# Performance work log

Hardware: AMD Instinct MI355X
Metric: run time of the kernel (lower is better)

Reference implementation:

```python
import jax, jax.numpy as jnp
import numpy as np

N = 100000        # nodes
E = 3200000       # edges
F_IN = 512        # node features
H = 64            # hidden (self.hidden)
C = 40            # num_class
CONF_R = 0.5      # global conf_r threshold ratio
EPS = 1e-8        # torch cosine_similarity eps


def setup_inputs() -> dict:
    key = jax.random.key(0)
    ks = jax.random.split(key, 8)
    x = jax.random.normal(ks[0], (N, F_IN), dtype=jnp.float32)
    edge_index = jax.random.randint(ks[1], (2, E), 0, N, dtype=jnp.int32)
    edge_weight = jax.random.uniform(ks[2], (E,), dtype=jnp.float32)
    l_u_edges = jax.random.uniform(ks[3], (E,), dtype=jnp.float32)
    w1 = jax.random.normal(ks[4], (F_IN, H), dtype=jnp.float32) / np.float32(np.sqrt(F_IN))
    b1 = jnp.zeros((H,), dtype=jnp.float32)
    w2 = jax.random.normal(ks[5], (H, C), dtype=jnp.float32) / np.float32(np.sqrt(H))
    b2 = jnp.zeros((C,), dtype=jnp.float32)
    return {"x": x, "edge_index": edge_index, "edge_weight": edge_weight,
            "l_u_edges": l_u_edges, "w1": w1, "b1": b1, "w2": w2, "b2": b2}


def _gcn_propagate(h, src, dst, deg_inv_sqrt):
    # GCNConv symmetric normalization with self-loops:
    # out[i] = sum_{j->i} h[j] / sqrt(deg_j * deg_i) + h[i] / deg_i
    norm = deg_inv_sqrt[src] * deg_inv_sqrt[dst]          # [E]
    agg = jax.ops.segment_sum(h[src] * norm[:, None], dst, num_segments=N)
    agg = agg + h * (deg_inv_sqrt * deg_inv_sqrt)[:, None]  # self-loop term
    return agg


def reference(x, edge_index, edge_weight, l_u_edges, w1, b1, w2, b2):
    src = edge_index[0]
    dst = edge_index[1]
    # degree with self-loops (GCNConv default add_self_loops=True, unit edge weight)
    deg = jax.ops.segment_sum(jnp.ones((E,), x.dtype), dst, num_segments=N) + 1.0
    deg_inv_sqrt = jax.lax.rsqrt(deg)

    # layer 1: linear -> propagate -> bias -> relu  (dropout treated as identity/eval)
    h1 = _gcn_propagate(x @ w1, src, dst, deg_inv_sqrt) + b1
    h1 = jax.nn.relu(h1)
    # layer 2
    x2 = _gcn_propagate(h1 @ w2, src, dst, deg_inv_sqrt) + b2   # [N, C]

    # loss path: top-k threshold on edge_weight
    n_cut = int(E * CONF_R)
    thresh = jnp.sort(edge_weight)[E - n_cut]   # n_cut-th largest value

    a = x2[src]                                  # [E, C] gather
    b = x2[dst]
    na = jnp.maximum(jnp.sqrt(jnp.sum(a * a, axis=1)), EPS)
    nb = jnp.maximum(jnp.sqrt(jnp.sum(b * b, axis=1)), EPS)
    cos = jnp.sum(a * b, axis=1) / (na * nb)
    cosine_sim = 1.0 - cos

    mask = edge_weight >= thresh
    l_prop = jnp.where(mask, cosine_sim, 1.0 - cosine_sim)
    l_edge = jnp.where(mask, edge_weight, 1.0 - edge_weight)
    l_loss = jnp.mean(l_edge * l_prop * l_u_edges)   # data_id != 5 -> mean

    return jax.nn.log_softmax(x2, axis=1), l_loss
```

## Files before the change

kernel.cpp:

```cpp
#include <hip/hip_runtime.h>

#define NN 100000
#define NE 3200000
#define FIN 512
#define FH 64
#define FC 40
#define KRANK 1600000u
#define HBLK 512
#define HBINS 2048
#define NBUCK 782
#define BPAD 1024
#define SBLK 500
#define EPB 6400
#define LEPT 4

typedef __attribute__((ext_vector_type(8))) short bf16x8;
typedef __attribute__((ext_vector_type(4))) float f32x4;

__device__ __forceinline__ unsigned f2b_rn(float x) {
    unsigned u = __float_as_uint(x);
    return (u + 0x7FFFu + ((u >> 16) & 1u)) >> 16;
}
__device__ __forceinline__ unsigned pack2(float x, float y) {
    return f2b_rn(x) | (f2b_rn(y) << 16);
}
__device__ __forceinline__ float2 unp2(unsigned u) {
    return make_float2(__uint_as_float(u << 16), __uint_as_float(u & 0xFFFF0000u));
}
__device__ __forceinline__ int dot4i8(unsigned a, unsigned b, int c) {
    c += ((int)(a << 24) >> 24) * ((int)(b << 24) >> 24);
    c += ((int)(a << 16) >> 24) * ((int)(b << 16) >> 24);
    c += ((int)(a << 8) >> 24) * ((int)(b << 8) >> 24);
    c += ((int)a >> 24) * ((int)b >> 24);
    return c;
}

__global__ __launch_bounds__(256) void bucket_count(const int* __restrict__ dstv,
                                                    unsigned* __restrict__ bcnt) {
    __shared__ unsigned bh[4 * BPAD];
    int tid = threadIdx.x, wv = tid >> 6;
    for (int i = tid; i < 4 * BPAD; i += 256) bh[i] = 0u;
    __syncthreads();
    int base = blockIdx.x * EPB;
    for (int t = tid; t < EPB; t += 256) {
        int b = dstv[base + t] >> 7;
        atomicAdd(&bh[wv * BPAD + b], 1u);
    }
    __syncthreads();
    for (int i = tid; i < BPAD; i += 256) {
        unsigned s = bh[i] + bh[BPAD + i] + bh[2 * BPAD + i] + bh[3 * BPAD + i];
        if (s) atomicAdd(&bcnt[i], s);
    }
}

__global__ __launch_bounds__(1024) void bucket_scan(const unsigned* __restrict__ bcnt,
                                                    unsigned* __restrict__ boff,
                                                    unsigned* __restrict__ bfill,
                                                    int* __restrict__ row_ptr) {
    __shared__ unsigned sc[1024];
    int tid = threadIdx.x;
    unsigned v = (tid < NBUCK) ? bcnt[tid] : 0u;
    sc[tid] = v;
    __syncthreads();
    for (int off = 1; off < 1024; off <<= 1) {
        unsigned t = (tid >= off) ? sc[tid - off] : 0u;
        __syncthreads();
        sc[tid] += t;
        __syncthreads();
    }
    unsigned excl = sc[tid] - v;
    boff[tid] = excl;
    bfill[tid] = excl;
    if (tid == 0) row_ptr[NN] = NE;
}

__global__ __launch_bounds__(256) void bucket_scatter(const int* __restrict__ srcv,
                                                      const int* __restrict__ dstv,
                                                      unsigned* __restrict__ bfill,
                                                      unsigned* __restrict__ bp) {
    __shared__ unsigned bh[4 * BPAD];
    __shared__ unsigned bbase[BPAD];
    __shared__ unsigned bfl[BPAD];
    int tid = threadIdx.x, wv = tid >> 6;
    for (int i = tid; i < 4 * BPAD; i += 256) bh[i] = 0u;
    __syncthreads();
    int base = blockIdx.x * EPB;
    for (int t = tid; t < EPB; t += 256) {
        int b = dstv[base + t] >> 7;
        atomicAdd(&bh[wv * BPAD + b], 1u);
    }
    __syncthreads();
    for (int i = tid; i < BPAD; i += 256) {
        unsigned s = bh[i] + bh[BPAD + i] + bh[2 * BPAD + i] + bh[3 * BPAD + i];
        bbase[i] = s ? atomicAdd(&bfill[i], s) : 0u;
        bfl[i] = 0u;
    }
    __syncthreads();
    for (int t = tid; t < EPB; t += 256) {
        int d = dstv[base + t];
        int b = d >> 7;
        unsigned r = atomicAdd(&bfl[b], 1u);
        unsigned pk = (unsigned)srcv[base + t] | ((unsigned)(d & 127) << 17);
        bp[bbase[b] + r] = pk;
    }
}

__global__ __launch_bounds__(256) void bucket_build(const unsigned* __restrict__ bp,
                                                    const unsigned* __restrict__ boff,
                                                    int* __restrict__ row_ptr,
                                                    float* __restrict__ dis,
                                                    int* __restrict__ csr_src) {
    __shared__ unsigned lh[4 * 128];
    __shared__ unsigned sc[128];
    __shared__ unsigned gbase[128];
    __shared__ unsigned fl2[128];
    int b = blockIdx.x, tid = threadIdx.x, wv = tid >> 6;
    unsigned e0 = boff[b], e1 = boff[b + 1];
    int ecnt = (int)(e1 - e0);
    for (int i = tid; i < 512; i += 256) lh[i] = 0u;
    __syncthreads();
    for (int t = tid; t < ecnt; t += 256) {
        unsigned lid = bp[e0 + t] >> 17;
        atomicAdd(&lh[wv * 128 + lid], 1u);
    }
    __syncthreads();
    unsigned deg = 0;
    if (tid < 128) {
        deg = lh[tid] + lh[128 + tid] + lh[256 + tid] + lh[384 + tid];
        sc[tid] = deg;
    }
    __syncthreads();
    for (int off = 1; off < 128; off <<= 1) {
        unsigned t = (tid >= off && tid < 128) ? sc[tid - off] : 0u;
        __syncthreads();
        if (tid < 128) sc[tid] += t;
        __syncthreads();
    }
    if (tid < 128) {
        unsigned excl = sc[tid] - deg;
        gbase[tid] = e0 + excl;
        fl2[tid] = 0u;
        int n = b * 128 + tid;
        if (n < NN) {
            row_ptr[n] = (int)(e0 + excl);
            dis[n] = rsqrtf((float)deg + 1.0f);
        }
    }
    __syncthreads();
    for (int t = tid; t < ecnt; t += 256) {
        unsigned v = bp[e0 + t];
        unsigned lid = v >> 17;
        unsigned r = atomicAdd(&fl2[lid], 1u);
        csr_src[gbase[lid] + r] = (int)(v & 0x1FFFFu);
    }
}

__global__ __launch_bounds__(256) void hist_pass(const float* __restrict__ ew,
                                                 const int* __restrict__ sel,
                                                 int stage,
                                                 unsigned* __restrict__ hist) {
    __shared__ unsigned lh[4 * HBINS];
    int tid = threadIdx.x, blk = blockIdx.x;
    int wv = tid >> 6;
    for (int i = tid; i < 4 * HBINS; i += 256) lh[i] = 0u;
    __syncthreads();
    unsigned m1 = 0, m2 = 0;
    if (stage == 1) m1 = (unsigned)sel[0];
    if (stage == 2) m2 = ((unsigned)sel[0] << 11) | (unsigned)sel[2];
    int base = blk * (NE / HBLK);
    for (int t = tid; t < NE / HBLK; t += 256) {
        unsigned bits = __float_as_uint(ew[base + t]);
        if (stage == 0) {
            atomicAdd(&lh[wv * HBINS + (bits >> 21)], 1u);
        } else if (stage == 1) {
            if ((bits >> 21) == m1) atomicAdd(&lh[wv * HBINS + ((bits >> 10) & 0x7FFu)], 1u);
        } else {
            if ((bits >> 10) == m2) atomicAdd(&lh[wv * HBINS + (bits & 0x3FFu)], 1u);
        }
    }
    __syncthreads();
    for (int i = tid; i < HBINS; i += 256) {
        unsigned s = lh[i] + lh[HBINS + i] + lh[2 * HBINS + i] + lh[3 * HBINS + i];
        if (s) atomicAdd(&hist[i], s);
    }
}

__global__ __launch_bounds__(1024) void select_stage(unsigned* __restrict__ hist,
                                                     int* __restrict__ sel, int stage,
                                                     float* __restrict__ thr) {
    __shared__ unsigned sc[1024];
    __shared__ unsigned runs;
    int tid = threadIdx.x;
    unsigned Kr = (stage == 0) ? KRANK : (unsigned)sel[2 * stage - 1];
    if (tid == 0) runs = 0;
    __syncthreads();
    for (int ch = 0; ch < 2; ++ch) {
        unsigned v = hist[ch * 1024 + tid];
        sc[tid] = v;
        __syncthreads();
        for (int off = 1; off < 1024; off <<= 1) {
            unsigned t = (tid >= off) ? sc[tid - off] : 0u;
            __syncthreads();
            sc[tid] += t;
            __syncthreads();
        }
        unsigned incl = sc[tid];
        unsigned base = runs;
        unsigned lo = base + incl - v, hi = base + incl;
        if (Kr >= lo && Kr < hi) {
            int b = ch * 1024 + tid;
            sel[2 * stage] = b;
            sel[2 * stage + 1] = (int)(Kr - lo);
            if (stage == 2) {
                unsigned bits = ((unsigned)sel[0] << 21) | ((unsigned)sel[2] << 10) | (unsigned)b;
                thr[0] = __uint_as_float(bits);
            }
        }
        __syncthreads();
        if (tid == 1023) runs = base + incl;
        __syncthreads();
    }
    hist[tid] = 0u;
    hist[1024 + tid] = 0u;
}

__global__ __launch_bounds__(256) void gemm1(const float* __restrict__ x,
                                             const float* __restrict__ w1,
                                             unsigned short* __restrict__ hb) {
    __shared__ unsigned sA[64 * 20];
    __shared__ unsigned sB[64 * 20];
    int tid = threadIdx.x;
    int wv = tid >> 6, lane = tid & 63;
    int quad = lane >> 4, l16 = lane & 15;
    int rowBase = blockIdx.x * 64;
    f32x4 acc[4] = {};
    for (int k0 = 0; k0 < FIN; k0 += 32) {
#pragma unroll
        for (int i = 0; i < 2; ++i) {
            int idx = tid + 256 * i;
            int m = idx >> 3, q = idx & 7;
            int gr = rowBase + m;
            float4 v = (gr < NN) ? *(const float4*)&x[(size_t)gr * FIN + k0 + 4 * q]
                                 : make_float4(0.f, 0.f, 0.f, 0.f);
            sA[m * 20 + 2 * q] = pack2(v.x, v.y);
            sA[m * 20 + 2 * q + 1] = pack2(v.z, v.w);
        }
#pragma unroll
        for (int i = 0; i < 4; ++i) {
            int idx = tid + 256 * i;
            int n = idx & 63, kk = idx >> 6;
            float a = w1[(size_t)(k0 + 2 * kk) * FH + n];
            float b = w1[(size_t)(k0 + 2 * kk + 1) * FH + n];
            sB[n * 20 + kk] = pack2(a, b);
        }
        __syncthreads();
        bf16x8 af = *(const bf16x8*)&sA[(wv * 16 + l16) * 20 + quad * 4];
#pragma unroll
        for (int c = 0; c < 4; ++c) {
            bf16x8 bfg = *(const bf16x8*)&sB[(c * 16 + l16) * 20 + quad * 4];
            acc[c] = __builtin_amdgcn_mfma_f32_16x16x32_bf16(af, bfg, acc[c], 0, 0, 0);
        }
        __syncthreads();
    }
#pragma unroll
    for (int r = 0; r < 4; ++r) {
        int row = rowBase + wv * 16 + quad * 4 + r;
        if (row < NN) {
#pragma unroll
            for (int c = 0; c < 4; ++c)
                hb[(size_t)row * FH + c * 16 + l16] = (unsigned short)f2b_rn(acc[c][r]);
        }
    }
}

__global__ __launch_bounds__(256) void agg_relu1(const unsigned* __restrict__ hbw,
                                                 const float* __restrict__ dis,
                                                 const int* __restrict__ row_ptr,
                                                 const int* __restrict__ csr_src,
                                                 const float* __restrict__ b1,
                                                 float* __restrict__ h1) {
    int wave = threadIdx.x >> 6, lane = threadIdx.x & 63;
    int n = blockIdx.x * 4 + wave;
    if (n >= NN) return;
    int g = lane >> 3, j = lane & 7;
    float dn = dis[n];
    int e0 = row_ptr[n], e1 = row_ptr[n + 1];
    int total = e1 - e0 + 1;
    const uint4* hb4 = (const uint4*)hbw;
    float2 a0 = {0.f, 0.f}, a1 = {0.f, 0.f}, a2 = {0.f, 0.f}, a3 = {0.f, 0.f};
    for (int it = 0; it < total; it += 16) {
        int iA = it + g;
        int iB = it + 8 + g;
        int sA = n;
        float wA = 0.f;
        if (iA == 0) {
            wA = dn * dn;
        } else if (iA < total) {
            sA = csr_src[e0 + iA - 1];
            wA = dis[sA] * dn;
        }
        int sB = n;
        float wB = 0.f;
        if (iB < total) {
            sB = csr_src[e0 + iB - 1];
            wB = dis[sB] * dn;
        }
        uint4 vA = make_uint4(0u, 0u, 0u, 0u);
        uint4 vB = make_uint4(0u, 0u, 0u, 0u);
        if (iA < total) vA = hb4[(size_t)sA * 8 + j];
        if (iB < total) vB = hb4[(size_t)sB * 8 + j];
        float2 t;
        t = unp2(vA.x); a0.x = fmaf(t.x, wA, a0.x); a0.y = fmaf(t.y, wA, a0.y);
        t = unp2(vA.y); a1.x = fmaf(t.x, wA, a1.x); a1.y = fmaf(t.y, wA, a1.y);
        t = unp2(vA.z); a2.x = fmaf(t.x, wA, a2.x); a2.y = fmaf(t.y, wA, a2.y);
        t = unp2(vA.w); a3.x = fmaf(t.x, wA, a3.x); a3.y = fmaf(t.y, wA, a3.y);
        t = unp2(vB.x); a0.x = fmaf(t.x, wB, a0.x); a0.y = fmaf(t.y, wB, a0.y);
        t = unp2(vB.y); a1.x = fmaf(t.x, wB, a1.x); a1.y = fmaf(t.y, wB, a1.y);
        t = unp2(vB.z); a2.x = fmaf(t.x, wB, a2.x); a2.y = fmaf(t.y, wB, a2.y);
        t = unp2(vB.w); a3.x = fmaf(t.x, wB, a3.x); a3.y = fmaf(t.y, wB, a3.y);
    }
#pragma unroll
    for (int m = 8; m < 64; m <<= 1) {
        a0.x += __shfl_xor(a0.x, m); a0.y += __shfl_xor(a0.y, m);
        a1.x += __shfl_xor(a1.x, m); a1.y += __shfl_xor(a1.y, m);
        a2.x += __shfl_xor(a2.x, m); a2.y += __shfl_xor(a2.y, m);
        a3.x += __shfl_xor(a3.x, m); a3.y += __shfl_xor(a3.y, m);
    }
    if (g == 0) {
        float4 blo = *(const float4*)&b1[j * 8];
        float4 bhi = *(const float4*)&b1[j * 8 + 4];
        float4 olo = make_float4(fmaxf(a0.x + blo.x, 0.f), fmaxf(a0.y + blo.y, 0.f),
                                 fmaxf(a1.x + blo.z, 0.f), fmaxf(a1.y + blo.w, 0.f));
        float4 ohi = make_float4(fmaxf(a2.x + bhi.x, 0.f), fmaxf(a2.y + bhi.y, 0.f),
                                 fmaxf(a3.x + bhi.z, 0.f), fmaxf(a3.y + bhi.w, 0.f));
        *(float4*)&h1[(size_t)n * FH + j * 8] = olo;
        *(float4*)&h1[(size_t)n * FH + j * 8 + 4] = ohi;
    }
}

__global__ __launch_bounds__(256) void gemm2(const float* __restrict__ h1,
                                             const float* __restrict__ w2,
                                             unsigned* __restrict__ h2w) {
    __shared__ float w2s[FH * FC];
    int tid = threadIdx.x;
    for (int i = tid; i < FH * FC; i += 256) w2s[i] = w2[i];
    __syncthreads();
    int wave = tid >> 6, lane = tid & 63;
    int n = blockIdx.x * 4 + wave;
    if (n >= NN) return;
    float hv = h1[(size_t)n * FH + lane];
    int cl = (lane < FC) ? lane : 0;
    float acc = 0.f;
#pragma unroll
    for (int k = 0; k < FH; ++k) {
        float xk = __shfl(hv, k);
        acc = fmaf(xk, w2s[k * FC + cl], acc);
    }
    float lo = __shfl(acc, 2 * lane);
    float hi = __shfl(acc, 2 * lane + 1);
    if (lane < 20) h2w[(size_t)n * 20 + lane] = pack2(lo, hi);
}

__global__ __launch_bounds__(256) void agg2_fused(const unsigned* __restrict__ h2w,
                                                  const float* __restrict__ dis,
                                                  const int* __restrict__ row_ptr,
                                                  const int* __restrict__ csr_src,
                                                  const float* __restrict__ b2,
                                                  unsigned* __restrict__ x2b,
                                                  float* __restrict__ outls) {
    int wave = threadIdx.x >> 6, lane = threadIdx.x & 63;
    int n = blockIdx.x * 4 + wave;
    if (n >= NN) return;
    int half = lane >> 5, li = lane & 31;
    bool ld = li < 20;
    int lidx = ld ? li : 19;
    float dn = dis[n];
    float2 acc = make_float2(0.f, 0.f);
    if (half == 0 && ld) {
        float2 v = unp2(h2w[(size_t)n * 20 + li]);
        float w = dn * dn;
        acc.x = v.x * w; acc.y = v.y * w;
    }
    int e0 = row_ptr[n], e1 = row_ptr[n + 1];
    int e = e0 + half;
    for (; e + 6 < e1; e += 8) {
        int s0 = csr_src[e], s1 = csr_src[e + 2];
        int s2 = csr_src[e + 4], s3 = csr_src[e + 6];
        float w0 = dis[s0] * dn, w1w = dis[s1] * dn;
        float w2w = dis[s2] * dn, w3w = dis[s3] * dn;
        float2 v0 = unp2(h2w[(size_t)s0 * 20 + lidx]);
        float2 v1 = unp2(h2w[(size_t)s1 * 20 + lidx]);
        float2 v2 = unp2(h2w[(size_t)s2 * 20 + lidx]);
        float2 v3 = unp2(h2w[(size_t)s3 * 20 + lidx]);
        if (ld) {
            acc.x = fmaf(v0.x, w0, acc.x); acc.y = fmaf(v0.y, w0, acc.y);
            acc.x = fmaf(v1.x, w1w, acc.x); acc.y = fmaf(v1.y, w1w, acc.y);
            acc.x = fmaf(v2.x, w2w, acc.x); acc.y = fmaf(v2.y, w2w, acc.y);
            acc.x = fmaf(v3.x, w3w, acc.x); acc.y = fmaf(v3.y, w3w, acc.y);
        }
    }
    for (; e + 2 < e1; e += 4) {
        int s0 = csr_src[e], s1 = csr_src[e + 2];
        float w0 = dis[s0] * dn, w1w = dis[s1] * dn;
        float2 v0 = unp2(h2w[(size_t)s0 * 20 + lidx]);
        float2 v1 = unp2(h2w[(size_t)s1 * 20 + lidx]);
        if (ld) {
            acc.x = fmaf(v0.x, w0, acc.x); acc.y = fmaf(v0.y, w0, acc.y);
            acc.x = fmaf(v1.x, w1w, acc.x); acc.y = fmaf(v1.y, w1w, acc.y);
        }
    }
    if (e < e1) {
        int s = csr_src[e];
        float w = dis[s] * dn;
        float2 v = unp2(h2w[(size_t)s * 20 + lidx]);
        if (ld) { acc.x = fmaf(v.x, w, acc.x); acc.y = fmaf(v.y, w, acc.y); }
    }
    float ax = acc.x + __shfl_xor(acc.x, 32);
    float ay = acc.y + __shfl_xor(acc.y, 32);
    bool actv = (half == 0) && ld;
    float2 x2v;
    if (actv) {
        float2 b = ((const float2*)b2)[li];
        x2v = make_float2(ax + b.x, ay + b.y);
    } else {
        x2v = make_float2(-3.4e38f, -3.4e38f);
    }
    float m = fmaxf(x2v.x, x2v.y);
#pragma unroll
    for (int off = 16; off; off >>= 1) m = fmaxf(m, __shfl_xor(m, off));
    float ex = actv ? (expf(x2v.x - m) + expf(x2v.y - m)) : 0.f;
    float sq = actv ? (x2v.x * x2v.x + x2v.y * x2v.y) : 0.f;
#pragma unroll
    for (int off = 16; off; off >>= 1) {
        ex += __shfl_xor(ex, off);
        sq += __shfl_xor(sq, off);
    }
    unsigned pk = 0;
    float inv = 0.f;
    if (actv) {
        inv = 127.f / fmaxf(sqrtf(sq), 1e-8f);
        int qx = (int)rintf(fminf(fmaxf(x2v.x * inv, -127.f), 127.f));
        int qy = (int)rintf(fminf(fmaxf(x2v.y * inv, -127.f), 127.f));
        pk = (unsigned)(qx & 0xFF) | ((unsigned)(qy & 0xFF) << 8);
    }
    unsigned wlo = __shfl(pk, (2 * lane) & 63);
    unsigned whi = __shfl(pk, (2 * lane + 1) & 63);
    unsigned wrd = wlo | (whi << 16);
    if (lane < 12) x2b[(size_t)n * 12 + lane] = wrd;
    if (actv) {
        float lse = m + logf(ex);
        *(float2*)&outls[(size_t)n * FC + 2 * li] = make_float2(x2v.x - lse, x2v.y - lse);
    }
}

__global__ __launch_bounds__(256) void loss_kernel(const int* __restrict__ srcv,
                                                   const int* __restrict__ dstv,
                                                   const float* __restrict__ ew,
                                                   const float* __restrict__ lu,
                                                   const unsigned* __restrict__ x2b,
                                                   const float* __restrict__ thr,
                                                   double* __restrict__ acc) {
    int base = blockIdx.x * (256 * LEPT) + threadIdx.x;
    float thr0 = thr[0];
    int s[LEPT], d[LEPT];
    float w[LEPT], l[LEPT];
#pragma unroll
    for (int i = 0; i < LEPT; ++i) {
        int e = base + i * 256;
        s[i] = srcv[e];
        d[i] = dstv[e];
        w[i] = ew[e];
        l[i] = lu[e];
    }
    uint4 A[LEPT][3], B[LEPT][3];
#pragma unroll
    for (int i = 0; i < LEPT; ++i) {
        const uint4* pa = (const uint4*)(x2b + (size_t)s[i] * 12);
        const uint4* pb = (const uint4*)(x2b + (size_t)d[i] * 12);
#pragma unroll
        for (int j = 0; j < 3; ++j) {
            A[i][j] = pa[j];
            B[i][j] = pb[j];
        }
    }
    float term = 0.f;
#pragma unroll
    for (int i = 0; i < LEPT; ++i) {
        int dot = 0;
#pragma unroll
        for (int j = 0; j < 3; ++j) {
            uint4 av = A[i][j], bv = B[i][j];
            dot = dot4i8(av.x, bv.x, dot);
            dot = dot4i8(av.y, bv.y, dot);
            dot = dot4i8(av.z, bv.z, dot);
            dot = dot4i8(av.w, bv.w, dot);
        }
        float cosv = (float)dot * (1.0f / 16129.0f);
        float cs = 1.f - cosv;
        bool mk = (w[i] >= thr0);
        float lp = mk ? cs : 1.f - cs;
        float le = mk ? w[i] : 1.f - w[i];
        term = fmaf(le * lp, l[i], term);
    }
#pragma unroll
    for (int off = 32; off; off >>= 1) term += __shfl_down(term, off);
    __shared__ float ws4[4];
    int lane = threadIdx.x & 63, wid = threadIdx.x >> 6;
    if (lane == 0) ws4[wid] = term;
    __syncthreads();
    if (threadIdx.x == 0) {
        double sm = (double)ws4[0] + (double)ws4[1] + (double)ws4[2] + (double)ws4[3];
        atomicAdd(acc, sm);
    }
}

__global__ void finalize(const double* __restrict__ acc, float* __restrict__ out) {
    out[NN * FC] = (float)(acc[0] * (1.0 / (double)NE));
}

extern "C" void kernel_launch(void* const* d_in, const int* in_sizes, int n_in,
                              void* d_out, int out_size, void* d_ws, size_t ws_size,
                              hipStream_t stream) {
    const float* x  = (const float*)d_in[0];
    const int*   ei = (const int*)d_in[1];
    const float* ew = (const float*)d_in[2];
    const float* lu = (const float*)d_in[3];
    const float* w1 = (const float*)d_in[4];
    const float* b1 = (const float*)d_in[5];
    const float* w2 = (const float*)d_in[6];
    const float* b2 = (const float*)d_in[7];
    float* out = (float*)d_out;
    const int* srcv = ei;
    const int* dstv = ei + NE;

    char* ws = (char*)d_ws;
    size_t off = 0;
    auto alloc = [&](size_t bytes) -> void* {
        void* p = ws + off;
        off += (bytes + 255) & ~(size_t)255;
        return p;
    };
    float*    dis     = (float*)alloc((size_t)NN * 4);
    int*      row_ptr = (int*)alloc((size_t)(NN + 1) * 4);
    int*      csr_src = (int*)alloc((size_t)NE * 4);
    unsigned* bp      = (unsigned*)alloc((size_t)NE * 4);
    unsigned* bcnt    = (unsigned*)alloc((size_t)BPAD * 4);
    unsigned* boff2   = (unsigned*)alloc((size_t)BPAD * 4);
    unsigned* bfill   = (unsigned*)alloc((size_t)BPAD * 4);
    unsigned short* hb = (unsigned short*)alloc((size_t)NN * FH * 2);
    float*    h1      = (float*)alloc((size_t)NN * FH * 4);
    unsigned* h2w     = (unsigned*)alloc((size_t)NN * 20 * 4);
    unsigned* x2b     = (unsigned*)alloc((size_t)NN * 12 * 4);
    unsigned* histr   = (unsigned*)alloc((size_t)HBINS * 4);
    int*      sel     = (int*)alloc(256);
    float*    thr     = (float*)alloc(256);
    double*   accd    = (double*)alloc(256);

    hipMemsetAsync(bcnt, 0, (size_t)BPAD * 4, stream);
    hipMemsetAsync(histr, 0, (size_t)HBINS * 4, stream);
    hipMemsetAsync(accd, 0, 8, stream);

    const int LB = NE / (256 * LEPT);
    const int NB4 = (NN + 3) / 4;

    bucket_count<<<SBLK, 256, 0, stream>>>(dstv, bcnt);
    bucket_scan<<<1, 1024, 0, stream>>>(bcnt, boff2, bfill, row_ptr);
    bucket_scatter<<<SBLK, 256, 0, stream>>>(srcv, dstv, bfill, bp);
    bucket_build<<<NBUCK, 256, 0, stream>>>(bp, boff2, row_ptr, dis, csr_src);

    hist_pass<<<HBLK, 256, 0, stream>>>(ew, sel, 0, histr);
    select_stage<<<1, 1024, 0, stream>>>(histr, sel, 0, thr);
    hist_pass<<<HBLK, 256, 0, stream>>>(ew, sel, 1, histr);
    select_stage<<<1, 1024, 0, stream>>>(histr, sel, 1, thr);
    hist_pass<<<HBLK, 256, 0, stream>>>(ew, sel, 2, histr);
    select_stage<<<1, 1024, 0, stream>>>(histr, sel, 2, thr);

    gemm1<<<(NN + 63) / 64, 256, 0, stream>>>(x, w1, hb);
    agg_relu1<<<NB4, 256, 0, stream>>>((const unsigned*)hb, dis, row_ptr, csr_src, b1, h1);
    gemm2<<<NB4, 256, 0, stream>>>(h1, w2, h2w);
    agg2_fused<<<NB4, 256, 0, stream>>>(h2w, dis, row_ptr, csr_src, b2, x2b, out);
    loss_kernel<<<LB, 256, 0, stream>>>(srcv, dstv, ew, lu, x2b, thr, accd);
    finalize<<<1, 1, 0, stream>>>(accd, out);
}
```

Before: 926.5 us.

## Restructure gemm1, widen aggregation unrolling, pad layer-2 features to 64-byte rows

gemm1 now stages all of w1 in shared memory once per block and loads x rows straight from global into MFMA operand registers. Each wave computes 32 rows with two accumulator sets, which removes the per-k-step shared staging of x and its barriers. The layer-1 aggregation now issues four neighbour gathers per iteration instead of two, for more memory-level parallelism. The layer-2 features are padded to 32 words (bf16) and 16 words (int8), so agg2 can reuse the same 8-lane uint4 gather pattern and the loss kernel can do aligned loads. This trades extra memory footprint and padded traffic for wider, aligned gathers.

```diff
diff --git a/kernel.cpp b/kernel.cpp
--- a/kernel.cpp
+++ b/kernel.cpp
@@ -227,48 +227,57 @@
 __global__ __launch_bounds__(256) void gemm1(const float* __restrict__ x,
                                              const float* __restrict__ w1,
                                              unsigned short* __restrict__ hb) {
-    __shared__ unsigned sA[64 * 20];
-    __shared__ unsigned sB[64 * 20];
+    __shared__ unsigned sB[64 * 260];
     int tid = threadIdx.x;
+    {
+        int col = tid & 63;
+        for (int kw = tid >> 6; kw < 256; kw += 4) {
+            float a = w1[(size_t)(2 * kw) * FH + col];
+            float b = w1[(size_t)(2 * kw + 1) * FH + col];
+            sB[col * 260 + kw] = pack2(a, b);
+        }
+    }
+    __syncthreads();
     int wv = tid >> 6, lane = tid & 63;
-    int quad = lane >> 4, l16 = lane & 15;
-    int rowBase = blockIdx.x * 64;
-    f32x4 acc[4] = {};
+    int l16 = lane & 15, quad = lane >> 4;
+    int r0 = blockIdx.x * 128 + wv * 32;
+    int rowA = r0 + l16, rowB = r0 + 16 + l16;
+    bool okA = rowA < NN, okB = rowB < NN;
+    const float* pA = x + (size_t)(okA ? rowA : 0) * FIN + quad * 8;
+    const float* pB = x + (size_t)(okB ? rowB : 0) * FIN + quad * 8;
+    f32x4 accA[4] = {};
+    f32x4 accB[4] = {};
     for (int k0 = 0; k0 < FIN; k0 += 32) {
-#pragma unroll
-        for (int i = 0; i < 2; ++i) {
-            int idx = tid + 256 * i;
-            int m = idx >> 3, q = idx & 7;
-            int gr = rowBase + m;
-            float4 v = (gr < NN) ? *(const float4*)&x[(size_t)gr * FIN + k0 + 4 * q]
-                                 : make_float4(0.f, 0.f, 0.f, 0.f);
-            sA[m * 20 + 2 * q] = pack2(v.x, v.y);
-            sA[m * 20 + 2 * q + 1] = pack2(v.z, v.w);
-        }
-#pragma unroll
-        for (int i = 0; i < 4; ++i) {
-            int idx = tid + 256 * i;
-            int n = idx & 63, kk = idx >> 6;
-            float a = w1[(size_t)(k0 + 2 * kk) * FH + n];
-            float b = w1[(size_t)(k0 + 2 * kk + 1) * FH + n];
-            sB[n * 20 + kk] = pack2(a, b);
-        }
-        __syncthreads();
-        bf16x8 af = *(const bf16x8*)&sA[(wv * 16 + l16) * 20 + quad * 4];
+        float4 xa0 = *(const float4*)(pA + k0);
+        float4 xa1 = *(const float4*)(pA + k0 + 4);
+        float4 xb0 = *(const float4*)(pB + k0);
+        float4 xb1 = *(const float4*)(pB + k0 + 4);
+        union { unsigned u[4]; bf16x8 v; } ca, cb;
+        ca.u[0] = pack2(xa0.x, xa0.y); ca.u[1] = pack2(xa0.z, xa0.w);
+        ca.u[2] = pack2(xa1.x, xa1.y); ca.u[3] = pack2(xa1.z, xa1.w);
+        cb.u[0] = pack2(xb0.x, xb0.y); cb.u[1] = pack2(xb0.z, xb0.w);
+        cb.u[2] = pack2(xb1.x, xb1.y); cb.u[3] = pack2(xb1.z, xb1.w);
+        int kwb = (k0 >> 1) + quad * 4;
 #pragma unroll
         for (int c = 0; c < 4; ++c) {
-            bf16x8 bfg = *(const bf16x8*)&sB[(c * 16 + l16) * 20 + quad * 4];
-            acc[c] = __builtin_amdgcn_mfma_f32_16x16x32_bf16(af, bfg, acc[c], 0, 0, 0);
-        }
-        __syncthreads();
+            bf16x8 bf = *(const bf16x8*)&sB[(c * 16 + l16) * 260 + kwb];
+            accA[c] = __builtin_amdgcn_mfma_f32_16x16x32_bf16(ca.v, bf, accA[c], 0, 0, 0);
+            accB[c] = __builtin_amdgcn_mfma_f32_16x16x32_bf16(cb.v, bf, accB[c], 0, 0, 0);
+        }
     }
 #pragma unroll
     for (int r = 0; r < 4; ++r) {
-        int row = rowBase + wv * 16 + quad * 4 + r;
-        if (row < NN) {
+        int rowc = r0 + quad * 4 + r;
+        if (rowc < NN) {
 #pragma unroll
             for (int c = 0; c < 4; ++c)
-                hb[(size_t)row * FH + c * 16 + l16] = (unsigned short)f2b_rn(acc[c][r]);
+                hb[(size_t)rowc * FH + c * 16 + l16] = (unsigned short)f2b_rn(accA[c][r]);
+        }
+        int rowd = r0 + 16 + quad * 4 + r;
+        if (rowd < NN) {
+#pragma unroll
+            for (int c = 0; c < 4; ++c)
+                hb[(size_t)rowd * FH + c * 16 + l16] = (unsigned short)f2b_rn(accB[c][r]);
         }
     }
 }
@@ -288,36 +297,30 @@
     int total = e1 - e0 + 1;
     const uint4* hb4 = (const uint4*)hbw;
     float2 a0 = {0.f, 0.f}, a1 = {0.f, 0.f}, a2 = {0.f, 0.f}, a3 = {0.f, 0.f};
-    for (int it = 0; it < total; it += 16) {
-        int iA = it + g;
-        int iB = it + 8 + g;
-        int sA = n;
-        float wA = 0.f;
-        if (iA == 0) {
-            wA = dn * dn;
-        } else if (iA < total) {
-            sA = csr_src[e0 + iA - 1];
-            wA = dis[sA] * dn;
-        }
-        int sB = n;
-        float wB = 0.f;
-        if (iB < total) {
-            sB = csr_src[e0 + iB - 1];
-            wB = dis[sB] * dn;
-        }
-        uint4 vA = make_uint4(0u, 0u, 0u, 0u);
-        uint4 vB = make_uint4(0u, 0u, 0u, 0u);
-        if (iA < total) vA = hb4[(size_t)sA * 8 + j];
-        if (iB < total) vB = hb4[(size_t)sB * 8 + j];
+    for (int it = 0; it < total; it += 32) {
+        int i0 = it + g, i1 = i0 + 8, i2 = i0 + 16, i3 = i0 + 24;
+        int s0 = n, s1 = n, s2 = n, s3 = n;
+        if (i0 > 0 && i0 < total) s0 = csr_src[e0 + i0 - 1];
+        if (i1 < total) s1 = csr_src[e0 + i1 - 1];
+        if (i2 < total) s2 = csr_src[e0 + i2 - 1];
+        if (i3 < total) s3 = csr_src[e0 + i3 - 1];
+        float w0 = (i0 < total) ? ((i0 == 0) ? dn * dn : dis[s0] * dn) : 0.f;
+        float w1_ = (i1 < total) ? dis[s1] * dn : 0.f;
+        float w2_ = (i2 < total) ? dis[s2] * dn : 0.f;
+        float w3_ = (i3 < total) ? dis[s3] * dn : 0.f;
+        uint4 z4 = make_uint4(0u, 0u, 0u, 0u);
+        uint4 v0 = z4, v1 = z4, v2 = z4, v3 = z4;
+        if (i0 < total) v0 = hb4[(size_t)s0 * 8 + j];
+        if (i1 < total) v1 = hb4[(size_t)s1 * 8 + j];
+        if (i2 < total) v2 = hb4[(size_t)s2 * 8 + j];
+        if (i3 < total) v3 = hb4[(size_t)s3 * 8 + j];
         float2 t;
-        t = unp2(vA.x); a0.x = fmaf(t.x, wA, a0.x); a0.y = fmaf(t.y, wA, a0.y);
-        t = unp2(vA.y); a1.x = fmaf(t.x, wA, a1.x); a1.y = fmaf(t.y, wA, a1.y);
-        t = unp2(vA.z); a2.x = fmaf(t.x, wA, a2.x); a2.y = fmaf(t.y, wA, a2.y);
-        t = unp2(vA.w); a3.x = fmaf(t.x, wA, a3.x); a3.y = fmaf(t.y, wA, a3.y);
-        t = unp2(vB.x); a0.x = fmaf(t.x, wB, a0.x); a0.y = fmaf(t.y, wB, a0.y);
-        t = unp2(vB.y); a1.x = fmaf(t.x, wB, a1.x); a1.y = fmaf(t.y, wB, a1.y);
-        t = unp2(vB.z); a2.x = fmaf(t.x, wB, a2.x); a2.y = fmaf(t.y, wB, a2.y);
-        t = unp2(vB.w); a3.x = fmaf(t.x, wB, a3.x); a3.y = fmaf(t.y, wB, a3.y);
+#define ACC8(V, W)                                                     \
+        t = unp2(V.x); a0.x = fmaf(t.x, W, a0.x); a0.y = fmaf(t.y, W, a0.y); \
+        t = unp2(V.y); a1.x = fmaf(t.x, W, a1.x); a1.y = fmaf(t.y, W, a1.y); \
+        t = unp2(V.z); a2.x = fmaf(t.x, W, a2.x); a2.y = fmaf(t.y, W, a2.y); \
+        t = unp2(V.w); a3.x = fmaf(t.x, W, a3.x); a3.y = fmaf(t.y, W, a3.y);
+        ACC8(v0, w0) ACC8(v1, w1_) ACC8(v2, w2_) ACC8(v3, w3_)
     }
 #pragma unroll
     for (int m = 8; m < 64; m <<= 1) {
@@ -356,9 +359,9 @@
         float xk = __shfl(hv, k);
         acc = fmaf(xk, w2s[k * FC + cl], acc);
     }
-    float lo = __shfl(acc, 2 * lane);
-    float hi = __shfl(acc, 2 * lane + 1);
-    if (lane < 20) h2w[(size_t)n * 20 + lane] = pack2(lo, hi);
+    float lo = __shfl(acc, (2 * lane) & 63);
+    float hi = __shfl(acc, (2 * lane + 1) & 63);
+    if (lane < 32) h2w[(size_t)n * 32 + lane] = (lane < 20) ? pack2(lo, hi) : 0u;
 }
 
 __global__ __launch_bounds__(256) void agg2_fused(const unsigned* __restrict__ h2w,
@@ -371,85 +374,87 @@
     int wave = threadIdx.x >> 6, lane = threadIdx.x & 63;
     int n = blockIdx.x * 4 + wave;
     if (n >= NN) return;
-    int half = lane >> 5, li = lane & 31;
-    bool ld = li < 20;
-    int lidx = ld ? li : 19;
+    int g = lane >> 3, j = lane & 7;
     float dn = dis[n];
-    float2 acc = make_float2(0.f, 0.f);
-    if (half == 0 && ld) {
-        float2 v = unp2(h2w[(size_t)n * 20 + li]);
-        float w = dn * dn;
-        acc.x = v.x * w; acc.y = v.y * w;
-    }
     int e0 = row_ptr[n], e1 = row_ptr[n + 1];
-    int e = e0 + half;
-    for (; e + 6 < e1; e += 8) {
-        int s0 = csr_src[e], s1 = csr_src[e + 2];
-        int s2 = csr_src[e + 4], s3 = csr_src[e + 6];
-        float w0 = dis[s0] * dn, w1w = dis[s1] * dn;
-        float w2w = dis[s2] * dn, w3w = dis[s3] * dn;
-        float2 v0 = unp2(h2w[(size_t)s0 * 20 + lidx]);
-        float2 v1 = unp2(h2w[(size_t)s1 * 20 + lidx]);
-        float2 v2 = unp2(h2w[(size_t)s2 * 20 + lidx]);
-        float2 v3 = unp2(h2w[(size_t)s3 * 20 + lidx]);
-        if (ld) {
-            acc.x = fmaf(v0.x, w0, acc.x); acc.y = fmaf(v0.y, w0, acc.y);
-            acc.x = fmaf(v1.x, w1w, acc.x); acc.y = fmaf(v1.y, w1w, acc.y);
-            acc.x = fmaf(v2.x, w2w, acc.x); acc.y = fmaf(v2.y, w2w, acc.y);
-            acc.x = fmaf(v3.x, w3w, acc.x); acc.y = fmaf(v3.y, w3w, acc.y);
-        }
-    }
-    for (; e + 2 < e1; e += 4) {
-        int s0 = csr_src[e], s1 = csr_src[e + 2];
-        float w0 = dis[s0] * dn, w1w = dis[s1] * dn;
-        float2 v0 = unp2(h2w[(size_t)s0 * 20 + lidx]);
-        float2 v1 = unp2(h2w[(size_t)s1 * 20 + lidx]);
-        if (ld) {
-            acc.x = fmaf(v0.x, w0, acc.x); acc.y = fmaf(v0.y, w0, acc.y);
-            acc.x = fmaf(v1.x, w1w, acc.x); acc.y = fmaf(v1.y, w1w, acc.y);
-        }
-    }
-    if (e < e1) {
-        int s = csr_src[e];
-        float w = dis[s] * dn;
-        float2 v = unp2(h2w[(size_t)s * 20 + lidx]);
-        if (ld) { acc.x = fmaf(v.x, w, acc.x); acc.y = fmaf(v.y, w, acc.y); }
-    }
-    float ax = acc.x + __shfl_xor(acc.x, 32);
-    float ay = acc.y + __shfl_xor(acc.y, 32);
-    bool actv = (half == 0) && ld;
-    float2 x2v;
-    if (actv) {
-        float2 b = ((const float2*)b2)[li];
-        x2v = make_float2(ax + b.x, ay + b.y);
-    } else {
-        x2v = make_float2(-3.4e38f, -3.4e38f);
-    }
-    float m = fmaxf(x2v.x, x2v.y);
-#pragma unroll
-    for (int off = 16; off; off >>= 1) m = fmaxf(m, __shfl_xor(m, off));
-    float ex = actv ? (expf(x2v.x - m) + expf(x2v.y - m)) : 0.f;
-    float sq = actv ? (x2v.x * x2v.x + x2v.y * x2v.y) : 0.f;
-#pragma unroll
-    for (int off = 16; off; off >>= 1) {
+    int total = e1 - e0 + 1;
+    const uint4* h4 = (const uint4*)h2w;
+    float2 a0 = {0.f, 0.f}, a1 = {0.f, 0.f}, a2 = {0.f, 0.f}, a3 = {0.f, 0.f};
+    for (int it = 0; it < total; it += 32) {
+        int i0 = it + g, i1 = i0 + 8, i2 = i0 + 16, i3 = i0 + 24;
+        int s0 = n, s1 = n, s2 = n, s3 = n;
+        if (i0 > 0 && i0 < total) s0 = csr_src[e0 + i0 - 1];
+        if (i1 < total) s1 = csr_src[e0 + i1 - 1];
+        if (i2 < total) s2 = csr_src[e0 + i2 - 1];
+        if (i3 < total) s3 = csr_src[e0 + i3 - 1];
+        float w0 = (i0 < total) ? ((i0 == 0) ? dn * dn : dis[s0] * dn) : 0.f;
+        float w1_ = (i1 < total) ? dis[s1] * dn : 0.f;
+        float w2_ = (i2 < total) ? dis[s2] * dn : 0.f;
+        float w3_ = (i3 < total) ? dis[s3] * dn : 0.f;
+        uint4 z4 = make_uint4(0u, 0u, 0u, 0u);
+        uint4 v0 = z4, v1 = z4, v2 = z4, v3 = z4;
+        if (i0 < total) v0 = h4[(size_t)s0 * 8 + j];
+        if (i1 < total) v1 = h4[(size_t)s1 * 8 + j];
+        if (i2 < total) v2 = h4[(size_t)s2 * 8 + j];
+        if (i3 < total) v3 = h4[(size_t)s3 * 8 + j];
+        float2 t;
+        ACC8(v0, w0) ACC8(v1, w1_) ACC8(v2, w2_) ACC8(v3, w3_)
+    }
+#pragma unroll
+    for (int m = 8; m < 64; m <<= 1) {
+        a0.x += __shfl_xor(a0.x, m); a0.y += __shfl_xor(a0.y, m);
+        a1.x += __shfl_xor(a1.x, m); a1.y += __shfl_xor(a1.y, m);
+        a2.x += __shfl_xor(a2.x, m); a2.y += __shfl_xor(a2.y, m);
+        a3.x += __shfl_xor(a3.x, m); a3.y += __shfl_xor(a3.y, m);
+    }
+    bool jv = (j < 5);
+    float4 blo = make_float4(0.f, 0.f, 0.f, 0.f), bhi = blo;
+    if (jv) {
+        blo = *(const float4*)&b2[j * 8];
+        bhi = *(const float4*)&b2[j * 8 + 4];
+    }
+    float c0 = a0.x + blo.x, c1 = a0.y + blo.y, c2 = a1.x + blo.z, c3 = a1.y + blo.w;
+    float c4 = a2.x + bhi.x, c5 = a2.y + bhi.y, c6 = a3.x + bhi.z, c7 = a3.y + bhi.w;
+    if (!jv) { c0 = c1 = c2 = c3 = c4 = c5 = c6 = c7 = -3.4e38f; }
+    float mx = fmaxf(fmaxf(fmaxf(c0, c1), fmaxf(c2, c3)),
+                     fmaxf(fmaxf(c4, c5), fmaxf(c6, c7)));
+#pragma unroll
+    for (int off = 1; off < 8; off <<= 1) mx = fmaxf(mx, __shfl_xor(mx, off));
+    float ex = 0.f, sq = 0.f;
+    if (jv) {
+        ex = expf(c0 - mx) + expf(c1 - mx) + expf(c2 - mx) + expf(c3 - mx)
+           + expf(c4 - mx) + expf(c5 - mx) + expf(c6 - mx) + expf(c7 - mx);
+        sq = c0 * c0 + c1 * c1 + c2 * c2 + c3 * c3 + c4 * c4 + c5 * c5 + c6 * c6 + c7 * c7;
+    }
+#pragma unroll
+    for (int off = 1; off < 8; off <<= 1) {
         ex += __shfl_xor(ex, off);
         sq += __shfl_xor(sq, off);
     }
-    unsigned pk = 0;
-    float inv = 0.f;
-    if (actv) {
-        inv = 127.f / fmaxf(sqrtf(sq), 1e-8f);
-        int qx = (int)rintf(fminf(fmaxf(x2v.x * inv, -127.f), 127.f));
-        int qy = (int)rintf(fminf(fmaxf(x2v.y * inv, -127.f), 127.f));
-        pk = (unsigned)(qx & 0xFF) | ((unsigned)(qy & 0xFF) << 8);
-    }
-    unsigned wlo = __shfl(pk, (2 * lane) & 63);
-    unsigned whi = __shfl(pk, (2 * lane + 1) & 63);
-    unsigned wrd = wlo | (whi << 16);
-    if (lane < 12) x2b[(size_t)n * 12 + lane] = wrd;
-    if (actv) {
-        float lse = m + logf(ex);
-        *(float2*)&outls[(size_t)n * FC + 2 * li] = make_float2(x2v.x - lse, x2v.y - lse);
+    if (g == 0) {
+        if (jv) {
+            float inv = 127.f / fmaxf(sqrtf(sq), 1e-8f);
+            int q0 = (int)rintf(fminf(fmaxf(c0 * inv, -127.f), 127.f));
+            int q1 = (int)rintf(fminf(fmaxf(c1 * inv, -127.f), 127.f));
+            int q2 = (int)rintf(fminf(fmaxf(c2 * inv, -127.f), 127.f));
+            int q3 = (int)rintf(fminf(fmaxf(c3 * inv, -127.f), 127.f));
+            int q4 = (int)rintf(fminf(fmaxf(c4 * inv, -127.f), 127.f));
+            int q5 = (int)rintf(fminf(fmaxf(c5 * inv, -127.f), 127.f));
+            int q6 = (int)rintf(fminf(fmaxf(c6 * inv, -127.f), 127.f));
+            int q7 = (int)rintf(fminf(fmaxf(c7 * inv, -127.f), 127.f));
+            unsigned qlo = (unsigned)(q0 & 255) | ((unsigned)(q1 & 255) << 8) |
+                           ((unsigned)(q2 & 255) << 16) | ((unsigned)(q3 & 255) << 24);
+            unsigned qhi = (unsigned)(q4 & 255) | ((unsigned)(q5 & 255) << 8) |
+                           ((unsigned)(q6 & 255) << 16) | ((unsigned)(q7 & 255) << 24);
+            *(uint2*)&x2b[(size_t)n * 16 + 2 * j] = make_uint2(qlo, qhi);
+            float lse = mx + logf(ex);
+            *(float4*)&outls[(size_t)n * FC + 8 * j] =
+                make_float4(c0 - lse, c1 - lse, c2 - lse, c3 - lse);
+            *(float4*)&outls[(size_t)n * FC + 8 * j + 4] =
+                make_float4(c4 - lse, c5 - lse, c6 - lse, c7 - lse);
+        } else {
+            *(uint2*)&x2b[(size_t)n * 16 + 2 * j] = make_uint2(0u, 0u);
+        }
     }
 }
 
@@ -472,15 +477,15 @@
         w[i] = ew[e];
         l[i] = lu[e];
     }
-    uint4 A[LEPT][3], B[LEPT][3];
+    uint4 A[LEPT][4], B[LEPT][4];
 #pragma unroll
     for (int i = 0; i < LEPT; ++i) {
-        const uint4* pa = (const uint4*)(x2b + (size_t)s[i] * 12);
-        const uint4* pb = (const uint4*)(x2b + (size_t)d[i] * 12);
-#pragma unroll
-        for (int j = 0; j < 3; ++j) {
-            A[i][j] = pa[j];
-            B[i][j] = pb[j];
+        const uint4* pa = (const uint4*)(x2b + (size_t)s[i] * 16);
+        const uint4* pb = (const uint4*)(x2b + (size_t)d[i] * 16);
+#pragma unroll
+        for (int jq = 0; jq < 4; ++jq) {
+            A[i][jq] = pa[jq];
+            B[i][jq] = pb[jq];
         }
     }
     float term = 0.f;
@@ -488,8 +493,8 @@
     for (int i = 0; i < LEPT; ++i) {
         int dot = 0;
 #pragma unroll
-        for (int j = 0; j < 3; ++j) {
-            uint4 av = A[i][j], bv = B[i][j];
+        for (int jq = 0; jq < 4; ++jq) {
+            uint4 av = A[i][jq], bv = B[i][jq];
             dot = dot4i8(av.x, bv.x, dot);
             dot = dot4i8(av.y, bv.y, dot);
             dot = dot4i8(av.z, bv.z, dot);
@@ -549,8 +554,8 @@
     unsigned* bfill   = (unsigned*)alloc((size_t)BPAD * 4);
     unsigned short* hb = (unsigned short*)alloc((size_t)NN * FH * 2);
     float*    h1      = (float*)alloc((size_t)NN * FH * 4);
-    unsigned* h2w     = (unsigned*)alloc((size_t)NN * 20 * 4);
-    unsigned* x2b     = (unsigned*)alloc((size_t)NN * 12 * 4);
+    unsigned* h2w     = (unsigned*)alloc((size_t)NN * 32 * 4);
+    unsigned* x2b     = (unsigned*)alloc((size_t)NN * 16 * 4);
     unsigned* histr   = (unsigned*)alloc((size_t)HBINS * 4);
     int*      sel     = (int*)alloc(256);
     float*    thr     = (float*)alloc(256);
@@ -575,7 +580,7 @@
     hist_pass<<<HBLK, 256, 0, stream>>>(ew, sel, 2, histr);
     select_stage<<<1, 1024, 0, stream>>>(histr, sel, 2, thr);
 
-    gemm1<<<(NN + 63) / 64, 256, 0, stream>>>(x, w1, hb);
+    gemm1<<<(NN + 127) / 128, 256, 0, stream>>>(x, w1, hb);
     agg_relu1<<<NB4, 256, 0, stream>>>((const unsigned*)hb, dis, row_ptr, csr_src, b1, h1);
     gemm2<<<NB4, 256, 0, stream>>>(h1, w2, h2w);
     agg2_fused<<<NB4, 256, 0, stream>>>(h2w, dis, row_ptr, csr_src, b2, x2b, out);
```

Result: faster. 878.3 us (-5.2%).
